# Kernel optimization log

Hardware: AMD Instinct MI355X
Metric: run time of the kernel (lower is better)

## Reference

```python
import jax, jax.numpy as jnp
import numpy as np

L, H, NH, HD, FF, S, B, V, NL = 2, 2048, 16, 128, 4096, 1024, 2, 32000, 4
R, SCALING, BLK = 2, 16.0 / 2.0, 64  # LoRA r=2, alpha=16 -> scaling 8; NF4 blocksize 64
NF4 = jnp.array([-1.0, -0.6961928009986877, -0.5250730514526367, -0.39491748809814453,
                 -0.28444138169288635, -0.18477343022823334, -0.09105003625154495, 0.0,
                 0.07958029955625534, 0.16093020141124725, 0.24611230194568634,
                 0.33791524171829224, 0.44070982933044434, 0.5626170039176941,
                 0.7229568362236023, 1.0], dtype=jnp.float32)

def dequant(codes, scales):
    # codes [out, in] int -> NF4 values; scales [out, in//BLK] absmax per 64-block
    return NF4[codes] * jnp.repeat(scales, BLK, axis=-1)

def qlin(x, codes, scales, A, Bm):
    # fused dequant + GEMM + LoRA low-rank update: x @ (Wd + s*B@A).T
    W = dequant(codes, scales)
    return x @ W.T + SCALING * ((x @ A.T) @ Bm.T)

def layer_norm(x, g, b):
    mu = jnp.mean(x, -1, keepdims=True)
    var = jnp.var(x, -1, keepdims=True)
    return (x - mu) * jax.lax.rsqrt(var + 1e-5) * g + b

def rope(x):  # x [B,S,NH,HD]
    half = HD // 2
    inv = 1.0 / (10000.0 ** (jnp.arange(half, dtype=jnp.float32) / half))
    ang = jnp.arange(S, dtype=jnp.float32)[:, None] * inv[None, :]
    cos = jnp.concatenate([jnp.cos(ang)] * 2, -1)[None, :, None, :]
    sin = jnp.concatenate([jnp.sin(ang)] * 2, -1)[None, :, None, :]
    x1, x2 = x[..., :half], x[..., half:]
    return x * cos + jnp.concatenate([-x2, x1], -1) * sin

def setup_inputs() -> dict:
    key = jax.random.key(0)
    it = iter(jax.random.split(key, 64))
    nrm = lambda shp, s: jax.random.normal(next(it), shp, jnp.float32) * s
    cod = lambda shp: jax.random.randint(next(it), shp, 0, 16, jnp.int32)
    scl = lambda shp: jax.random.uniform(next(it), shp, jnp.float32) * 0.02 + 1e-3
    lens = jax.random.randint(next(it), (B,), S // 2, S + 1)
    return dict(
        input_ids=jax.random.randint(next(it), (B, S), 0, V, jnp.int32),
        attention_mask=(jnp.arange(S)[None, :] < lens[:, None]).astype(jnp.int32),
        labels=jax.random.randint(next(it), (B,), 0, NL, jnp.int32),
        embed=nrm((V, H), 0.02),
        qkv_codes=cod((L, 3 * H, H)), qkv_scales=scl((L, 3 * H, H // BLK)),
        qkv_A=nrm((L, R, H), 0.01), qkv_B=nrm((L, 3 * H, R), 0.01),
        dense_codes=cod((L, H, H)), dense_scales=scl((L, H, H // BLK)),
        dense_A=nrm((L, R, H), 0.01), dense_B=nrm((L, H, R), 0.01),
        min_codes=cod((L, 2 * FF, H)), min_scales=scl((L, 2 * FF, H // BLK)),
        min_A=nrm((L, R, H), 0.01), min_B=nrm((L, 2 * FF, R), 0.01),
        mout_codes=cod((L, H, FF)), mout_scales=scl((L, H, FF // BLK)),
        mout_A=nrm((L, R, FF), 0.01), mout_B=nrm((L, H, R), 0.01),
        ln1_g=jnp.ones((L, H)), ln1_b=jnp.zeros((L, H)),
        ln2_g=jnp.ones((L, H)), ln2_b=jnp.zeros((L, H)),
        lnf_g=jnp.ones((H,)), lnf_b=jnp.zeros((H,)),
        classifier_w=nrm((NL, H), 0.01),
    )

def reference(input_ids, attention_mask, labels, embed, qkv_codes, qkv_scales, qkv_A, qkv_B,
              dense_codes, dense_scales, dense_A, dense_B, min_codes, min_scales, min_A, min_B,
              mout_codes, mout_scales, mout_A, mout_B, ln1_g, ln1_b, ln2_g, ln2_b,
              lnf_g, lnf_b, classifier_w):
    x = embed[input_ids]  # [B,S,H]
    mask = jnp.tril(jnp.ones((S, S), bool))[None, None] & (attention_mask[:, None, None, :] > 0)
    for l in range(L):
        h = layer_norm(x, ln1_g[l], ln1_b[l])
        qkv = qlin(h, qkv_codes[l], qkv_scales[l], qkv_A[l], qkv_B[l]).reshape(B, S, NH, 3 * HD)
        q, k, v = qkv[..., :HD], qkv[..., HD:2 * HD], qkv[..., 2 * HD:]
        q, k = rope(q), rope(k)
        scores = jnp.einsum('bqhd,bkhd->bhqk', q, k) / np.float32(np.sqrt(HD))
        probs = jax.nn.softmax(jnp.where(mask, scores, jnp.float32(-1e30)), -1)
        attn = jnp.einsum('bhqk,bkhd->bqhd', probs, v).reshape(B, S, H)
        x = x + qlin(attn, dense_codes[l], dense_scales[l], dense_A[l], dense_B[l])
        h2 = layer_norm(x, ln2_g[l], ln2_b[l])
        u = qlin(h2, min_codes[l], min_scales[l], min_A[l], min_B[l])  # [B,S,2*FF] packed SwiGLU
        g = jax.nn.silu(u[..., :FF]) * u[..., FF:]
        x = x + qlin(g, mout_codes[l], mout_scales[l], mout_A[l], mout_B[l])
    x = layer_norm(x, lnf_g, lnf_b)
    eos = x[jnp.arange(B), attention_mask.sum(1) - 1]  # last non-padded token hidden
    logits = eos @ classifier_w.T
    logp = jax.nn.log_softmax(logits, -1)
    loss = -jnp.mean(logp[jnp.arange(B), labels])
    return loss, logits
```

## Files before the change

### kernel.cpp

```cpp
#include <hip/hip_runtime.h>

typedef unsigned short u16;
typedef __attribute__((ext_vector_type(4))) float f32x4;
typedef __attribute__((ext_vector_type(8))) short short8;
typedef __attribute__((ext_vector_type(4))) short short4v;

constexpr int CL  = 2;
constexpr int CH  = 2048;
constexpr int CNH = 16;
constexpr int CHD = 128;
constexpr int CFF = 4096;
constexpr int CS  = 1024;
constexpr int CB  = 2;
constexpr int CNL = 4;
constexpr int CM  = CB * CS;
#define SCALING 8.0f

__device__ __constant__ float NF4TAB[16] = {
    -1.0f, -0.6961928009986877f, -0.5250730514526367f, -0.39491748809814453f,
    -0.28444138169288635f, -0.18477343022823334f, -0.09105003625154495f, 0.0f,
    0.07958029955625534f, 0.16093020141124725f, 0.24611230194568634f,
    0.33791524171829224f, 0.44070982933044434f, 0.5626170039176941f,
    0.7229568362236023f, 1.0f};

__device__ __forceinline__ u16 f2bf(float f) {
  union { float f; unsigned u; } v; v.f = f;
  unsigned r = v.u + 0x7fffu + ((v.u >> 16) & 1u);
  return (u16)(r >> 16);
}
__device__ __forceinline__ float bf2f(u16 u) {
  union { unsigned u; float f; } v; v.u = ((unsigned)u) << 16;
  return v.f;
}

template <int N> __device__ __forceinline__ void wait_vm() {
  if constexpr (N == 0)      asm volatile("s_waitcnt vmcnt(0)" ::: "memory");
  else if constexpr (N == 6) asm volatile("s_waitcnt vmcnt(6)" ::: "memory");
  else if constexpr (N == 8) asm volatile("s_waitcnt vmcnt(8)" ::: "memory");
  else                       asm volatile("s_waitcnt vmcnt(0)" ::: "memory");
}

__device__ __forceinline__ float blockReduceSum(float v) {
  __shared__ float sh[4];
  #pragma unroll
  for (int o = 32; o > 0; o >>= 1) v += __shfl_down(v, o);
  __syncthreads();
  if ((threadIdx.x & 63) == 0) sh[threadIdx.x >> 6] = v;
  __syncthreads();
  return sh[0] + sh[1] + sh[2] + sh[3];
}

__global__ void k_embed(const int* __restrict__ ids, const float* __restrict__ emb,
                        float* __restrict__ x) {
  int m = blockIdx.x;
  const float4* src = (const float4*)(emb + (size_t)ids[m] * CH);
  float4* dst = (float4*)(x + (size_t)m * CH);
  for (int i = threadIdx.x; i < CH / 4; i += 256) dst[i] = src[i];
}

__global__ void k_ln_xa(const float* __restrict__ x, const float* __restrict__ g,
                        const float* __restrict__ b, const float* __restrict__ A,
                        u16* __restrict__ o, float* __restrict__ xA) {
  int m = blockIdx.x, tid = threadIdx.x;
  const float* row = x + (size_t)m * CH;
  float s = 0.f, s2 = 0.f;
  for (int i = tid; i < CH / 4; i += 256) {
    float4 v = ((const float4*)row)[i];
    s += v.x + v.y + v.z + v.w;
    s2 += v.x * v.x + v.y * v.y + v.z * v.z + v.w * v.w;
  }
  s = blockReduceSum(s);
  s2 = blockReduceSum(s2);
  float mu = s / CH, var = s2 / CH - mu * mu;
  float rs = rsqrtf(var + 1e-5f);
  u16* orow = o + (size_t)m * CH;
  float s0 = 0.f, s1 = 0.f;
  for (int i = tid; i < CH / 4; i += 256) {
    float4 v = ((const float4*)row)[i];
    float4 gv = ((const float4*)g)[i];
    float4 bv = ((const float4*)b)[i];
    float4 a0 = ((const float4*)A)[i];
    float4 a1 = ((const float4*)(A + CH))[i];
    float h0 = (v.x - mu) * rs * gv.x + bv.x;
    float h1 = (v.y - mu) * rs * gv.y + bv.y;
    float h2 = (v.z - mu) * rs * gv.z + bv.z;
    float h3 = (v.w - mu) * rs * gv.w + bv.w;
    short4v ov = { (short)f2bf(h0), (short)f2bf(h1), (short)f2bf(h2), (short)f2bf(h3) };
    *(short4v*)(orow + i * 4) = ov;
    s0 += h0 * a0.x + h1 * a0.y + h2 * a0.z + h3 * a0.w;
    s1 += h0 * a1.x + h1 * a1.y + h2 * a1.z + h3 * a1.w;
  }
  s0 = blockReduceSum(s0);
  s1 = blockReduceSum(s1);
  if (tid == 0) { xA[2 * m] = s0; xA[2 * m + 1] = s1; }
}

__global__ void k_xa(const u16* __restrict__ xb, const float* __restrict__ A,
                     float* __restrict__ xA, int K) {
  int m = blockIdx.x, tid = threadIdx.x;
  const u16* row = xb + (size_t)m * K;
  float s0 = 0.f, s1 = 0.f;
  for (int c = tid; c < K / 8; c += 256) {
    short8 v = *(const short8*)(row + c * 8);
    #pragma unroll
    for (int e = 0; e < 8; ++e) {
      float f = bf2f((u16)v[e]);
      s0 += f * A[c * 8 + e];
      s1 += f * A[K + c * 8 + e];
    }
  }
  s0 = blockReduceSum(s0);
  s1 = blockReduceSum(s1);
  if (tid == 0) { xA[2 * m] = s0; xA[2 * m + 1] = s1; }
}

__global__ void k_dequant(const int* __restrict__ codes, const float* __restrict__ scales,
                          u16* __restrict__ w, int kshift, long total) {
  __shared__ float lut[16];
  if (threadIdx.x < 16) lut[threadIdx.x] = NF4TAB[threadIdx.x];
  __syncthreads();
  long base = ((long)blockIdx.x * 256 + threadIdx.x) * 8;
  if (base >= total) return;
  long n = base >> kshift;
  int k = (int)(base & ((1L << kshift) - 1));
  float sc = scales[(size_t)n * (1 << (kshift - 6)) + (k >> 6)];
  const int* cp = codes + base;
  short8 o;
  #pragma unroll
  for (int i = 0; i < 8; ++i) o[i] = (short)f2bf(lut[cp[i] & 15] * sc);
  *(short8*)(w + base) = o;
}

__global__ void k_ropetab(float* __restrict__ cosT, float* __restrict__ sinT) {
  int i = blockIdx.x * 256 + threadIdx.x;
  if (i >= CS * 64) return;
  int s = i >> 6, d = i & 63;
  float inv = powf(10000.0f, -(float)d / 64.0f);
  float a = (float)s * inv;
  cosT[i] = cosf(a);
  sinT[i] = sinf(a);
}

__global__ void k_rope(const u16* __restrict__ qkv, const float* __restrict__ cosT,
                       const float* __restrict__ sinT, u16* __restrict__ Qb,
                       u16* __restrict__ Kb) {
  int bid = blockIdx.x;
  int s = bid & (CS - 1);
  int z = bid >> 10;
  int b = z >> 4, h = z & 15;
  int d = threadIdx.x;
  const u16* base = qkv + ((size_t)(b * CS + s)) * (3 * CH) + h * (3 * CHD);
  int dh = d & 63;
  float c = cosT[s * 64 + dh], sn = sinT[s * 64 + dh];
  float sgn = (d < 64) ? -1.0f : 1.0f;
  float q = bf2f(base[d]),       qp = bf2f(base[d ^ 64]);
  float k = bf2f(base[CHD + d]), kp = bf2f(base[CHD + (d ^ 64)]);
  size_t oi = ((size_t)z * CS + s) * CHD + d;
  Qb[oi] = f2bf(q * c + sgn * qp * sn);
  Kb[oi] = f2bf(k * c + sgn * kp * sn);
}

__global__ void k_vtrans(const u16* __restrict__ qkv, u16* __restrict__ Vt) {
  __shared__ u16 tile[32][33];
  int z = blockIdx.z;
  int b = z >> 4, h = z & 15;
  int s0 = blockIdx.x * 32, d0 = blockIdx.y * 32;
  int tx = threadIdx.x, ty = threadIdx.y;
  #pragma unroll
  for (int i = 0; i < 32; i += 8)
    tile[ty + i][tx] =
        qkv[((size_t)(b * CS + s0 + ty + i)) * (3 * CH) + h * (3 * CHD) + 2 * CHD + d0 + tx];
  __syncthreads();
  #pragma unroll
  for (int i = 0; i < 32; i += 8)
    Vt[((size_t)z * CHD + d0 + ty + i) * CS + s0 + tx] = tile[tx][ty + i];
}

__global__ __launch_bounds__(256, 2) void k_flash(
    const u16* __restrict__ Qb, const u16* __restrict__ Kb, const u16* __restrict__ Vt,
    const int* __restrict__ amask, u16* __restrict__ out) {
  __shared__ u16 Ks[64 * 128];
  __shared__ u16 Vs[128 * 64];
  __shared__ float bias[CS];
  __shared__ u16 Ps[4][16][80];
  int bid = blockIdx.x;
  int qt = 15 - (bid >> 5);
  int z = bid & 31;
  int b = z >> 4, h = z & 15;
  int tid = threadIdx.x, lane = tid & 63, wid = tid >> 6;
  int lrow = lane & 15, lgrp = lane >> 4;
  const u16* Qz = Qb + (size_t)z * CS * CHD;
  const u16* Kz = Kb + (size_t)z * CS * CHD;
  const u16* Vz = Vt + (size_t)z * CHD * CS;

  for (int i = tid; i < CS; i += 256)
    bias[i] = amask[b * CS + i] ? 0.f : -1e30f;

  int qrow = qt * 64 + wid * 16 + lrow;
  short8 qf[4];
  #pragma unroll
  for (int kk = 0; kk < 4; ++kk)
    qf[kk] = *(const short8*)(Qz + (size_t)qrow * CHD + kk * 32 + lgrp * 8);

  float m_r[4], l_r[4];
  #pragma unroll
  for (int r = 0; r < 4; ++r) { m_r[r] = -3e38f; l_r[r] = 0.f; }
  f32x4 o_acc[8];
  #pragma unroll
  for (int dj = 0; dj < 8; ++dj) o_acc[dj] = (f32x4){0.f, 0.f, 0.f, 0.f};

  const float SCL = 0.08838834764831845f;

  for (int t = 0; t <= qt; ++t) {
    int k0 = t * 64;
    __syncthreads();
    #pragma unroll
    for (int it = 0; it < 4; ++it) {
      int c = it * 256 + tid;
      int key = c >> 4, ch = c & 15;
      short8 v = *(const short8*)(Kz + (size_t)(k0 + key) * CHD + ch * 8);
      *(short8*)((char*)Ks + key * 256 + ((ch * 16) ^ ((key & 7) << 4))) = v;
    }
    #pragma unroll
    for (int it = 0; it < 4; ++it) {
      int c = it * 256 + tid;
      int d = c >> 3, ch = c & 7;
      short8 v = *(const short8*)(Vz + (size_t)d * CS + k0 + ch * 8);
      *(short8*)((char*)Vs + d * 128 + ((ch * 16) ^ ((d & 7) << 4))) = v;
    }
    __syncthreads();

    f32x4 s_acc[4];
    #pragma unroll
    for (int nj = 0; nj < 4; ++nj) s_acc[nj] = (f32x4){0.f, 0.f, 0.f, 0.f};
    #pragma unroll
    for (int kk = 0; kk < 4; ++kk) {
      #pragma unroll
      for (int nj = 0; nj < 4; ++nj) {
        int key = nj * 16 + lrow;
        short8 kf = *(const short8*)((const char*)Ks + key * 256 +
                                     (((kk * 32 + lgrp * 8) * 2) ^ ((key & 7) << 4)));
        s_acc[nj] = __builtin_amdgcn_mfma_f32_16x16x32_bf16(qf[kk], kf, s_acc[nj], 0, 0, 0);
      }
    }

    bool diag = (t == qt);
    float p[4][4], mx[4];
    #pragma unroll
    for (int r = 0; r < 4; ++r) {
      int ql = wid * 16 + 4 * lgrp + r;
      float rm = -3e38f;
      #pragma unroll
      for (int nj = 0; nj < 4; ++nj) {
        int kl = nj * 16 + lrow;
        float v = s_acc[nj][r] * SCL + bias[k0 + kl];
        if (diag && kl > ql) v = -1e30f;
        p[nj][r] = v;
        rm = fmaxf(rm, v);
      }
      mx[r] = rm;
    }
    #pragma unroll
    for (int o = 1; o < 16; o <<= 1)
      #pragma unroll
      for (int r = 0; r < 4; ++r) mx[r] = fmaxf(mx[r], __shfl_xor(mx[r], o));
    float ps[4], alpha[4];
    #pragma unroll
    for (int r = 0; r < 4; ++r) {
      float mn = fmaxf(m_r[r], mx[r]);
      alpha[r] = __expf(m_r[r] - mn);
      m_r[r] = mn;
      float acc = 0.f;
      #pragma unroll
      for (int nj = 0; nj < 4; ++nj) {
        float e = __expf(p[nj][r] - mn);
        p[nj][r] = e;
        acc += e;
      }
      ps[r] = acc;
    }
    #pragma unroll
    for (int o = 1; o < 16; o <<= 1)
      #pragma unroll
      for (int r = 0; r < 4; ++r) ps[r] += __shfl_xor(ps[r], o);
    #pragma unroll
    for (int r = 0; r < 4; ++r) {
      l_r[r] = l_r[r] * alpha[r] + ps[r];
      #pragma unroll
      for (int dj = 0; dj < 8; ++dj) o_acc[dj][r] *= alpha[r];
    }

    #pragma unroll
    for (int r = 0; r < 4; ++r)
      #pragma unroll
      for (int nj = 0; nj < 4; ++nj)
        Ps[wid][4 * lgrp + r][nj * 16 + lrow] = f2bf(p[nj][r]);
    #pragma unroll
    for (int kk2 = 0; kk2 < 2; ++kk2) {
      short8 pa = *(const short8*)(&Ps[wid][lrow][kk2 * 32 + lgrp * 8]);
      #pragma unroll
      for (int dj = 0; dj < 8; ++dj) {
        int d = dj * 16 + lrow;
        short8 vf = *(const short8*)((const char*)Vs + d * 128 +
                                     (((kk2 * 32 + lgrp * 8) * 2) ^ ((d & 7) << 4)));
        o_acc[dj] = __builtin_amdgcn_mfma_f32_16x16x32_bf16(pa, vf, o_acc[dj], 0, 0, 0);
      }
    }
  }

  #pragma unroll
  for (int r = 0; r < 4; ++r) {
    float inv = 1.0f / l_r[r];
    int qg = qt * 64 + wid * 16 + 4 * lgrp + r;
    size_t rowoff = ((size_t)(b * CS + qg)) * CH + h * CHD;
    #pragma unroll
    for (int dj = 0; dj < 8; ++dj)
      out[rowoff + dj * 16 + lrow] = f2bf(o_acc[dj][r] * inv);
  }
}

__global__ void k_silu_xa(const u16* __restrict__ u, const float* __restrict__ A,
                          u16* __restrict__ g, float* __restrict__ xA) {
  int m = blockIdx.x, tid = threadIdx.x;
  const u16* urow = u + (size_t)m * (2 * CFF);
  u16* grow = g + (size_t)m * CFF;
  float s0 = 0.f, s1 = 0.f;
  for (int c = tid; c < CFF / 8; c += 256) {
    short8 va = *(const short8*)(urow + c * 8);
    short8 vb = *(const short8*)(urow + CFF + c * 8);
    short8 og;
    #pragma unroll
    for (int e = 0; e < 8; ++e) {
      float a = bf2f((u16)va[e]);
      float bb = bf2f((u16)vb[e]);
      float gg = (a / (1.0f + __expf(-a))) * bb;
      og[e] = (short)f2bf(gg);
      s0 += gg * A[c * 8 + e];
      s1 += gg * A[CFF + c * 8 + e];
    }
    *(short8*)(grow + c * 8) = og;
  }
  s0 = blockReduceSum(s0);
  s1 = blockReduceSum(s1);
  if (tid == 0) { xA[2 * m] = s0; xA[2 * m + 1] = s1; }
}

template <int BM, int BN, int TW, int WM, int WN, int OUT_BF16, int LORA, int RESID>
__global__ __launch_bounds__(TW, 2) void k_gemm3(
    const u16* __restrict__ Ag, const u16* __restrict__ Bg, void* __restrict__ Cout,
    const float* __restrict__ resid, const float* __restrict__ xA,
    const float* __restrict__ lB, int K, int N) {
  constexpr int WROWS = BM / WM, WCOLS = BN / WN;
  constexpr int M_REP = WROWS / 16, N_REP = WCOLS / 16;
  constexpr int LA = BM * 8 / TW, LBN = BN * 8 / TW;
  constexpr int LPT = LA + LBN;
  __shared__ __align__(16) u16 As[2][BM * 64];
  __shared__ __align__(16) u16 Bs[2][BN * 64];
  int tid = threadIdx.x, lane = tid & 63, wid = tid >> 6;
  int wm = wid / WN, wn = wid % WN;
  int gx = gridDim.x, nwg = gx * gridDim.y;
  int bid = blockIdx.y * gx + blockIdx.x;
  int qq = nwg >> 3, rr = nwg & 7;
  int xcd = bid & 7, lid = bid >> 3;
  int swz = (xcd < rr ? xcd * (qq + 1) : rr * (qq + 1) + (xcd - rr) * qq) + lid;
  long bm = (long)(swz % gx) * BM, bn = (long)(swz / gx) * BN;

  f32x4 acc[M_REP][N_REP];
  #pragma unroll
  for (int i = 0; i < M_REP; ++i)
    #pragma unroll
    for (int j = 0; j < N_REP; ++j) acc[i][j] = (f32x4){0.f, 0.f, 0.f, 0.f};

  auto stage = [&](int buf, int t) {
    int k0 = t * 64;
    #pragma unroll
    for (int i = 0; i < LA; ++i) {
      int f = i * TW + tid;
      int r = f >> 3, g = (f & 7) ^ (r & 7);
      __builtin_amdgcn_global_load_lds(
          (const __attribute__((address_space(1))) void*)(Ag + (size_t)(bm + r) * K + k0 + g * 8),
          (__attribute__((address_space(3))) void*)(&As[buf][f * 8]), 16, 0, 0);
    }
    #pragma unroll
    for (int i = 0; i < LBN; ++i) {
      int f = i * TW + tid;
      int r = f >> 3, g = (f & 7) ^ (r & 7);
      __builtin_amdgcn_global_load_lds(
          (const __attribute__((address_space(1))) void*)(Bg + (size_t)(bn + r) * K + k0 + g * 8),
          (__attribute__((address_space(3))) void*)(&Bs[buf][f * 8]), 16, 0, 0);
    }
  };

  int NT = K >> 6;
  stage(0, 0);
  stage(1, 1);

  int kg = lane >> 4, lr = lane & 15;
  for (int t = 0; t < NT; ++t) {
    int buf = t & 1;
    if (t + 1 < NT) wait_vm<LPT>();
    else            wait_vm<0>();
    __builtin_amdgcn_s_barrier();

    short8 af[2][M_REP], bfr[2][N_REP];
    #pragma unroll
    for (int kk = 0; kk < 2; ++kk) {
      int au = kk * 4 + kg;
      #pragma unroll
      for (int i = 0; i < M_REP; ++i) {
        int r = wm * WROWS + i * 16 + lr;
        af[kk][i] = *(const short8*)(&As[buf][r * 64 + ((au ^ (r & 7)) << 3)]);
      }
      #pragma unroll
      for (int j = 0; j < N_REP; ++j) {
        int r = wn * WCOLS + j * 16 + lr;
        bfr[kk][j] = *(const short8*)(&Bs[buf][r * 64 + ((au ^ (r & 7)) << 3)]);
      }
    }
    asm volatile("s_waitcnt lgkmcnt(0)" ::: "memory");
    __builtin_amdgcn_s_barrier();
    if (t + 2 < NT) stage(buf, t + 2);

    __builtin_amdgcn_s_setprio(1);
    #pragma unroll
    for (int kk = 0; kk < 2; ++kk)
      #pragma unroll
      for (int i = 0; i < M_REP; ++i)
        #pragma unroll
        for (int j = 0; j < N_REP; ++j)
          acc[i][j] = __builtin_amdgcn_mfma_f32_16x16x32_bf16(af[kk][i], bfr[kk][j], acc[i][j], 0, 0, 0);
    __builtin_amdgcn_s_setprio(0);
  }

  #pragma unroll
  for (int i = 0; i < M_REP; ++i) {
    #pragma unroll
    for (int r = 0; r < 4; ++r) {
      long m = bm + wm * WROWS + i * 16 + ((lane >> 4) << 2) + r;
      float xa0 = 0.f, xa1 = 0.f;
      if (LORA) { xa0 = xA[2 * m]; xa1 = xA[2 * m + 1]; }
      #pragma unroll
      for (int j = 0; j < N_REP; ++j) {
        long n = bn + wn * WCOLS + j * 16 + (lane & 15);
        float v = acc[i][j][r];
        if (LORA) v += SCALING * (xa0 * lB[2 * n] + xa1 * lB[2 * n + 1]);
        if (RESID) v += resid[m * N + n];
        if (OUT_BF16)
          ((u16*)Cout)[m * N + n] = f2bf(v);
        else
          ((float*)Cout)[m * N + n] = v;
      }
    }
  }
}

#define RD_A(d, mh)                                                              \
  { _Pragma("unroll") for (int kk = 0; kk < 2; ++kk) {                           \
      _Pragma("unroll") for (int ii = 0; ii < 4; ++ii) {                         \
        int ra = ((mh) * 4 + ii) * 16 + lr;                                      \
        int slot = (kk * 4 + kg) ^ ((lr >> 1) & 3);                              \
        a_f[kk][ii] = *(const short8*)(&As[d][wm][ra * 64 + slot * 8]);          \
      } } }
#define RD_B(d, nh)                                                              \
  { _Pragma("unroll") for (int kk = 0; kk < 2; ++kk) {                           \
      _Pragma("unroll") for (int jj = 0; jj < 2; ++jj) {                         \
        int rb = (wn & 1) * 64 + ((nh) * 2 + jj) * 16 + lr;                      \
        int slot = (kk * 4 + kg) ^ ((lr >> 1) & 3);                              \
        b_f[nh][kk][jj] = *(const short8*)(&Bs[d][wn >> 1][rb * 64 + slot * 8]); \
      } } }
#define MFMA_Q(mh, nh)                                                           \
  { __builtin_amdgcn_s_setprio(1);                                               \
    _Pragma("unroll") for (int kk = 0; kk < 2; ++kk) {                           \
      _Pragma("unroll") for (int ii = 0; ii < 4; ++ii) {                         \
        _Pragma("unroll") for (int jj = 0; jj < 2; ++jj) {                       \
          acc[(mh) * 4 + ii][(nh) * 2 + jj] =                                    \
              __builtin_amdgcn_mfma_f32_16x16x32_bf16(                           \
                  a_f[kk][ii], b_f[nh][kk][jj],                                  \
                  acc[(mh) * 4 + ii][(nh) * 2 + jj], 0, 0, 0);                   \
        } } }                                                                    \
    __builtin_amdgcn_s_setprio(0); }
#define LGKM0_SB                                                                 \
  asm volatile("s_waitcnt lgkmcnt(0)" ::: "memory");                             \
  __builtin_amdgcn_sched_barrier(0);
#define BAR __builtin_amdgcn_s_barrier();

__global__ __launch_bounds__(512, 2) void k_gemm8(
    const u16* __restrict__ Ag, const u16* __restrict__ Bg, u16* __restrict__ Cout,
    const float* __restrict__ xA, const float* __restrict__ lB, int K, int N) {
  __shared__ __align__(16) u16 As[2][2][128 * 64];
  __shared__ __align__(16) u16 Bs[2][2][128 * 64];
  int tid = threadIdx.x, lane = tid & 63, wid = tid >> 6;
  int wm = wid >> 2, wn = wid & 3;
  int kg = lane >> 4, lr = lane & 15;
  int gx = gridDim.x, nwg = gx * gridDim.y;
  int bid = blockIdx.y * gx + blockIdx.x;
  int qq = nwg >> 3, rr = nwg & 7;
  int xcd = bid & 7, lid = bid >> 3;
  int swz = (xcd < rr ? xcd * (qq + 1) : rr * (qq + 1) + (xcd - rr) * qq) + lid;
  long bm = (long)(swz % gx) * 256, bn = (long)(swz / gx) * 256;
  const int NKT = K >> 6;

  f32x4 acc[8][4];
  #pragma unroll
  for (int i = 0; i < 8; ++i)
    #pragma unroll
    for (int j = 0; j < 4; ++j) acc[i][j] = (f32x4){0.f, 0.f, 0.f, 0.f};
  short8 a_f[2][4], b_f[2][2][2];

  auto stA = [&](int t, int h) {
    int d = t & 1;
    int tt = t < NKT ? t : NKT - 1;
    int k0 = tt << 6;
    #pragma unroll
    for (int ld = 0; ld < 2; ++ld) {
      int f = ld * 512 + tid;
      int row = f >> 3, p = f & 7;
      int ss = p ^ ((row >> 1) & 3);
      __builtin_amdgcn_global_load_lds(
          (const __attribute__((address_space(1))) void*)(Ag + (size_t)(bm + h * 128 + row) * K + k0 + ss * 8),
          (__attribute__((address_space(3))) void*)(&As[d][h][f * 8]), 16, 0, 0);
    }
  };
  auto stB = [&](int t, int h) {
    int d = t & 1;
    int tt = t < NKT ? t : NKT - 1;
    int k0 = tt << 6;
    #pragma unroll
    for (int ld = 0; ld < 2; ++ld) {
      int f = ld * 512 + tid;
      int row = f >> 3, p = f & 7;
      int ss = p ^ ((row >> 1) & 3);
      __builtin_amdgcn_global_load_lds(
          (const __attribute__((address_space(1))) void*)(Bg + (size_t)(bn + h * 128 + row) * K + k0 + ss * 8),
          (__attribute__((address_space(3))) void*)(&Bs[d][h][f * 8]), 16, 0, 0);
    }
  };

  stA(0, 0); stA(0, 1); stB(0, 0); stB(0, 1);
  stB(1, 0); stA(1, 0);
  asm volatile("s_waitcnt vmcnt(4)" ::: "memory");
  BAR

  int NI = NKT >> 1;
  for (int j = 0; j < NI; ++j) {
    int t0 = 2 * j;
    RD_A(0, 0) RD_B(0, 0)
    stA(t0 + 1, 1);
    BAR LGKM0_SB MFMA_Q(0, 0) BAR
    RD_B(0, 1)
    stB(t0 + 1, 1);
    BAR LGKM0_SB MFMA_Q(0, 1) BAR
    RD_A(0, 1)
    stB(t0 + 2, 0);
    BAR LGKM0_SB MFMA_Q(1, 0) BAR
    stA(t0 + 2, 0);
    asm volatile("s_waitcnt vmcnt(2)" ::: "memory");
    BAR MFMA_Q(1, 1) BAR
    RD_A(1, 0) RD_B(1, 0)
    stA(t0 + 2, 1);
    BAR LGKM0_SB MFMA_Q(0, 0) BAR
    RD_B(1, 1)
    stB(t0 + 2, 1);
    BAR LGKM0_SB MFMA_Q(0, 1) BAR
    RD_A(1, 1)
    stB(t0 + 3, 0);
    BAR LGKM0_SB MFMA_Q(1, 0) BAR
    stA(t0 + 3, 0);
    asm volatile("s_waitcnt vmcnt(2)" ::: "memory");
    BAR MFMA_Q(1, 1) BAR
  }

  #pragma unroll
  for (int i = 0; i < 8; ++i) {
    #pragma unroll
    for (int r = 0; r < 4; ++r) {
      long m = bm + wm * 128 + i * 16 + ((lane >> 4) << 2) + r;
      float xa0 = xA[2 * m], xa1 = xA[2 * m + 1];
      #pragma unroll
      for (int j = 0; j < 4; ++j) {
        long n = bn + wn * 64 + j * 16 + (lane & 15);
        float v = acc[i][j][r] + SCALING * (xa0 * lB[2 * n] + xa1 * lB[2 * n + 1]);
        Cout[m * N + n] = f2bf(v);
      }
    }
  }
}

__global__ void k_final(const float* __restrict__ x, const int* __restrict__ amask,
                        const int* __restrict__ labels, const float* __restrict__ g,
                        const float* __restrict__ bb, const float* __restrict__ cw,
                        float* __restrict__ out) {
  __shared__ float xr[CH];
  __shared__ float lg[CB][CNL];
  int tid = threadIdx.x;
  for (int b = 0; b < CB; ++b) {
    float fc = 0.f;
    for (int k = tid; k < CS; k += 256) fc += (amask[b * CS + k] != 0) ? 1.0f : 0.0f;
    int len = (int)(blockReduceSum(fc) + 0.5f);
    const float* row = x + ((size_t)b * CS + (len - 1)) * CH;
    float s = 0.f, s2 = 0.f;
    for (int k = tid; k < CH; k += 256) { float v = row[k]; s += v; s2 += v * v; }
    s = blockReduceSum(s);
    s2 = blockReduceSum(s2);
    float mu = s / CH, var = s2 / CH - mu * mu;
    float rs = rsqrtf(var + 1e-5f);
    for (int k = tid; k < CH; k += 256) xr[k] = (row[k] - mu) * rs * g[k] + bb[k];
    __syncthreads();
    for (int c = 0; c < CNL; ++c) {
      float p = 0.f;
      for (int k = tid; k < CH; k += 256) p += xr[k] * cw[c * CH + k];
      p = blockReduceSum(p);
      if (tid == 0) { lg[b][c] = p; out[1 + b * CNL + c] = p; }
    }
    __syncthreads();
  }
  if (tid == 0) {
    float loss = 0.f;
    for (int b = 0; b < CB; ++b) {
      float mx = -1e30f;
      for (int c = 0; c < CNL; ++c) mx = fmaxf(mx, lg[b][c]);
      float se = 0.f;
      for (int c = 0; c < CNL; ++c) se += expf(lg[b][c] - mx);
      float lse = mx + logf(se);
      loss -= (lg[b][labels[b]] - lse);
    }
    out[0] = loss / CB;
  }
}

static constexpr size_t X_OFF  = 0;
static constexpr size_t H_OFF  = X_OFF + (size_t)CM * CH * 4;
static constexpr size_t W_OFF  = H_OFF + (size_t)CM * CH * 2;
static constexpr size_t SC_OFF = W_OFF + (size_t)8192 * 2048 * 2;
static constexpr size_t PR_OFF = SC_OFF + (size_t)32 * CS * CS * 4;
static constexpr size_t XA_OFF = PR_OFF + (size_t)32 * CS * CS * 2;
static constexpr size_t CS_OFF = XA_OFF + (size_t)CM * 2 * 4;
static constexpr size_t SN_OFF = CS_OFF + (size_t)CS * 64 * 4;
static constexpr size_t WS_END = SN_OFF + (size_t)CS * 64 * 4;

extern "C" void kernel_launch(void* const* d_in, const int* in_sizes, int n_in,
                              void* d_out, int out_size, void* d_ws, size_t ws_size,
                              hipStream_t stream) {
  (void)in_sizes; (void)n_in; (void)out_size;
  if (ws_size < WS_END) return;

  const int*   ids          = (const int*)d_in[0];
  const int*   amask        = (const int*)d_in[1];
  const int*   labels       = (const int*)d_in[2];
  const float* emb          = (const float*)d_in[3];
  const int*   qkv_codes    = (const int*)d_in[4];
  const float* qkv_scales   = (const float*)d_in[5];
  const float* qkv_A        = (const float*)d_in[6];
  const float* qkv_B        = (const float*)d_in[7];
  const int*   dense_codes  = (const int*)d_in[8];
  const float* dense_scales = (const float*)d_in[9];
  const float* dense_A      = (const float*)d_in[10];
  const float* dense_B      = (const float*)d_in[11];
  const int*   min_codes    = (const int*)d_in[12];
  const float* min_scales   = (const float*)d_in[13];
  const float* min_A        = (const float*)d_in[14];
  const float* min_B        = (const float*)d_in[15];
  const int*   mout_codes   = (const int*)d_in[16];
  const float* mout_scales  = (const float*)d_in[17];
  const float* mout_A       = (const float*)d_in[18];
  const float* mout_B       = (const float*)d_in[19];
  const float* ln1_g        = (const float*)d_in[20];
  const float* ln1_b        = (const float*)d_in[21];
  const float* ln2_g        = (const float*)d_in[22];
  const float* ln2_b        = (const float*)d_in[23];
  const float* lnf_g        = (const float*)d_in[24];
  const float* lnf_b        = (const float*)d_in[25];
  const float* cw           = (const float*)d_in[26];

  char* ws = (char*)d_ws;
  float* x       = (float*)(ws + X_OFF);
  u16*   hbuf    = (u16*)(ws + H_OFF);
  u16*   wbuf    = (u16*)(ws + W_OFF);
  u16*   Qb      = (u16*)(ws + W_OFF);
  u16*   Kb      = (u16*)(ws + W_OFF + (size_t)32 * CS * CHD * 2);
  u16*   Vt      = (u16*)(ws + W_OFF + (size_t)64 * CS * CHD * 2);
  u16*   qkv_out = (u16*)(ws + SC_OFF);
  u16*   ubuf    = (u16*)(ws + SC_OFF);
  u16*   gbuf    = (u16*)(ws + PR_OFF);
  float* xA      = (float*)(ws + XA_OFF);
  float* cosT    = (float*)(ws + CS_OFF);
  float* sinT    = (float*)(ws + SN_OFF);

  k_ropetab<<<(CS * 64 + 255) / 256, 256, 0, stream>>>(cosT, sinT);
  k_embed<<<CM, 256, 0, stream>>>(ids, emb, x);

  for (int l = 0; l < CL; ++l) {
    k_ln_xa<<<CM, 256, 0, stream>>>(x, ln1_g + l * CH, ln1_b + l * CH,
                                    qkv_A + (size_t)l * 2 * CH, hbuf, xA);
    long nq = (long)3 * CH * CH;
    k_dequant<<<(int)(nq / 8 / 256), 256, 0, stream>>>(
        qkv_codes + (size_t)l * nq, qkv_scales + (size_t)l * 3 * CH * (CH / 64),
        wbuf, 11, nq);
    k_gemm8<<<dim3(CM / 256, (3 * CH) / 256), 512, 0, stream>>>(
        hbuf, wbuf, qkv_out, xA, qkv_B + (size_t)l * 3 * CH * 2, CH, 3 * CH);
    k_rope<<<32 * CS, 128, 0, stream>>>(qkv_out, cosT, sinT, Qb, Kb);
    k_vtrans<<<dim3(CS / 32, CHD / 32, 32), dim3(32, 8), 0, stream>>>(qkv_out, Vt);
    k_flash<<<512, 256, 0, stream>>>(Qb, Kb, Vt, amask, hbuf);
    k_xa<<<CM, 256, 0, stream>>>(hbuf, dense_A + (size_t)l * 2 * CH, xA, CH);
    long nd = (long)CH * CH;
    k_dequant<<<(int)(nd / 8 / 256), 256, 0, stream>>>(
        dense_codes + (size_t)l * nd, dense_scales + (size_t)l * CH * (CH / 64),
        wbuf, 11, nd);
    k_gemm3<128, 64, 256, 2, 2, 0, 1, 1><<<dim3(CM / 128, CH / 64), 256, 0, stream>>>(
        hbuf, wbuf, x, x, xA, dense_B + (size_t)l * CH * 2, CH, CH);

    k_ln_xa<<<CM, 256, 0, stream>>>(x, ln2_g + l * CH, ln2_b + l * CH,
                                    min_A + (size_t)l * 2 * CH, hbuf, xA);
    long nm = (long)2 * CFF * CH;
    k_dequant<<<(int)(nm / 8 / 256), 256, 0, stream>>>(
        min_codes + (size_t)l * nm, min_scales + (size_t)l * 2 * CFF * (CH / 64),
        wbuf, 11, nm);
    k_gemm8<<<dim3(CM / 256, (2 * CFF) / 256), 512, 0, stream>>>(
        hbuf, wbuf, ubuf, xA, min_B + (size_t)l * 2 * CFF * 2, CH, 2 * CFF);
    k_silu_xa<<<CM, 256, 0, stream>>>(ubuf, mout_A + (size_t)l * 2 * CFF, gbuf, xA);
    long no = (long)CH * CFF;
    k_dequant<<<(int)(no / 8 / 256), 256, 0, stream>>>(
        mout_codes + (size_t)l * no, mout_scales + (size_t)l * CH * (CFF / 64),
        wbuf, 12, no);
    k_gemm3<128, 64, 256, 2, 2, 0, 1, 1><<<dim3(CM / 128, CH / 64), 256, 0, stream>>>(
        gbuf, wbuf, x, x, xA, mout_B + (size_t)l * CH * 2, CFF, CH);
  }

  k_final<<<1, 256, 0, stream>>>(x, amask, labels, lnf_g, lnf_b, cw, (float*)d_out);
}
```

Measured before the change: 775.1 us.

## Prefetch flash K/V tiles in registers, retune GEMM swizzle and waits, swap QKV GEMM

The flash attention kernel now loads the next K/V tile into registers while computing the current one, so global loads overlap the MFMA work. The gemm8 LDS swizzle changes to XOR with row&7, which is meant to reduce bank conflicts. Its vmcnt waits are relaxed from 2 to 4 to keep more loads in flight. The QKV projection switches from gemm8 to the templated gemm3 with 128x128 tiles. Together these add register pressure in flash, and the relaxed waits risk correctness if outstanding-load counts are miscounted.

Result: faster. 750.9 us (-3.1%).

```diff
diff --git a/kernel.cpp b/kernel.cpp
--- a/kernel.cpp
+++ b/kernel.cpp
@@ -211,6 +211,14 @@
 
   const float SCL = 0.08838834764831845f;
 
+  short8 kA[4], vA[4];
+  #pragma unroll
+  for (int it = 0; it < 4; ++it) {
+    int c = it * 256 + tid;
+    kA[it] = *(const short8*)(Kz + (size_t)(c >> 4) * CHD + (c & 15) * 8);
+    vA[it] = *(const short8*)(Vz + (size_t)(c >> 3) * CS + (c & 7) * 8);
+  }
+
   for (int t = 0; t <= qt; ++t) {
     int k0 = t * 64;
     __syncthreads();
@@ -218,15 +226,19 @@
     for (int it = 0; it < 4; ++it) {
       int c = it * 256 + tid;
       int key = c >> 4, ch = c & 15;
-      short8 v = *(const short8*)(Kz + (size_t)(k0 + key) * CHD + ch * 8);
-      *(short8*)((char*)Ks + key * 256 + ((ch * 16) ^ ((key & 7) << 4))) = v;
-    }
-    #pragma unroll
-    for (int it = 0; it < 4; ++it) {
-      int c = it * 256 + tid;
-      int d = c >> 3, ch = c & 7;
-      short8 v = *(const short8*)(Vz + (size_t)d * CS + k0 + ch * 8);
-      *(short8*)((char*)Vs + d * 128 + ((ch * 16) ^ ((d & 7) << 4))) = v;
+      *(short8*)((char*)Ks + key * 256 + ((ch * 16) ^ ((key & 7) << 4))) = kA[it];
+      int d = c >> 3, ch2 = c & 7;
+      *(short8*)((char*)Vs + d * 128 + ((ch2 * 16) ^ ((d & 7) << 4))) = vA[it];
+    }
+    short8 kB[4], vB[4];
+    if (t < qt) {
+      int k1 = k0 + 64;
+      #pragma unroll
+      for (int it = 0; it < 4; ++it) {
+        int c = it * 256 + tid;
+        kB[it] = *(const short8*)(Kz + (size_t)(k1 + (c >> 4)) * CHD + (c & 15) * 8);
+        vB[it] = *(const short8*)(Vz + (size_t)(c >> 3) * CS + k1 + (c & 7) * 8);
+      }
     }
     __syncthreads();
 
@@ -305,6 +317,11 @@
                                      (((kk2 * 32 + lgrp * 8) * 2) ^ ((d & 7) << 4)));
         o_acc[dj] = __builtin_amdgcn_mfma_f32_16x16x32_bf16(pa, vf, o_acc[dj], 0, 0, 0);
       }
+    }
+
+    if (t < qt) {
+      #pragma unroll
+      for (int it = 0; it < 4; ++it) { kA[it] = kB[it]; vA[it] = vB[it]; }
     }
   }
 
@@ -458,14 +475,14 @@
   { _Pragma("unroll") for (int kk = 0; kk < 2; ++kk) {                           \
       _Pragma("unroll") for (int ii = 0; ii < 4; ++ii) {                         \
         int ra = ((mh) * 4 + ii) * 16 + lr;                                      \
-        int slot = (kk * 4 + kg) ^ ((lr >> 1) & 3);                              \
+        int slot = (kk * 4 + kg) ^ (ra & 7);                                     \
         a_f[kk][ii] = *(const short8*)(&As[d][wm][ra * 64 + slot * 8]);          \
       } } }
 #define RD_B(d, nh)                                                              \
   { _Pragma("unroll") for (int kk = 0; kk < 2; ++kk) {                           \
       _Pragma("unroll") for (int jj = 0; jj < 2; ++jj) {                         \
         int rb = (wn & 1) * 64 + ((nh) * 2 + jj) * 16 + lr;                      \
-        int slot = (kk * 4 + kg) ^ ((lr >> 1) & 3);                              \
+        int slot = (kk * 4 + kg) ^ (rb & 7);                                     \
         b_f[nh][kk][jj] = *(const short8*)(&Bs[d][wn >> 1][rb * 64 + slot * 8]); \
       } } }
 #define MFMA_Q(mh, nh)                                                           \
@@ -515,7 +532,7 @@
     for (int ld = 0; ld < 2; ++ld) {
       int f = ld * 512 + tid;
       int row = f >> 3, p = f & 7;
-      int ss = p ^ ((row >> 1) & 3);
+      int ss = p ^ (row & 7);
       __builtin_amdgcn_global_load_lds(
           (const __attribute__((address_space(1))) void*)(Ag + (size_t)(bm + h * 128 + row) * K + k0 + ss * 8),
           (__attribute__((address_space(3))) void*)(&As[d][h][f * 8]), 16, 0, 0);
@@ -529,7 +546,7 @@
     for (int ld = 0; ld < 2; ++ld) {
       int f = ld * 512 + tid;
       int row = f >> 3, p = f & 7;
-      int ss = p ^ ((row >> 1) & 3);
+      int ss = p ^ (row & 7);
       __builtin_amdgcn_global_load_lds(
           (const __attribute__((address_space(1))) void*)(Bg + (size_t)(bn + h * 128 + row) * K + k0 + ss * 8),
           (__attribute__((address_space(3))) void*)(&Bs[d][h][f * 8]), 16, 0, 0);
@@ -554,7 +571,7 @@
     stB(t0 + 2, 0);
     BAR LGKM0_SB MFMA_Q(1, 0) BAR
     stA(t0 + 2, 0);
-    asm volatile("s_waitcnt vmcnt(2)" ::: "memory");
+    asm volatile("s_waitcnt vmcnt(4)" ::: "memory");
     BAR MFMA_Q(1, 1) BAR
     RD_A(1, 0) RD_B(1, 0)
     stA(t0 + 2, 1);
@@ -566,7 +583,7 @@
     stB(t0 + 3, 0);
     BAR LGKM0_SB MFMA_Q(1, 0) BAR
     stA(t0 + 3, 0);
-    asm volatile("s_waitcnt vmcnt(2)" ::: "memory");
+    asm volatile("s_waitcnt vmcnt(4)" ::: "memory");
     BAR MFMA_Q(1, 1) BAR
   }
 
@@ -696,8 +713,8 @@
     k_dequant<<<(int)(nq / 8 / 256), 256, 0, stream>>>(
         qkv_codes + (size_t)l * nq, qkv_scales + (size_t)l * 3 * CH * (CH / 64),
         wbuf, 11, nq);
-    k_gemm8<<<dim3(CM / 256, (3 * CH) / 256), 512, 0, stream>>>(
-        hbuf, wbuf, qkv_out, xA, qkv_B + (size_t)l * 3 * CH * 2, CH, 3 * CH);
+    k_gemm3<128, 128, 256, 2, 2, 1, 1, 0><<<dim3(CM / 128, (3 * CH) / 128), 256, 0, stream>>>(
+        hbuf, wbuf, qkv_out, nullptr, xA, qkv_B + (size_t)l * 3 * CH * 2, CH, 3 * CH);
     k_rope<<<32 * CS, 128, 0, stream>>>(qkv_out, cosT, sinT, Qb, Kb);
     k_vtrans<<<dim3(CS / 32, CHD / 32, 32), dim3(32, 8), 0, stream>>>(qkv_out, Vt);
     k_flash<<<512, 256, 0, stream>>>(Qb, Kb, Vt, amask, hbuf);
```
